# Kernel tuning notes

Measured on AMD Instinct MI355X. Metric: run time of the kernel, lower is better.

## Reference

```python
import jax, jax.numpy as jnp
import numpy as np

B, L, HID = 4, 1024, 1024
H, D = 16, 64  # num heads, head size


def setup_inputs() -> dict:
    key = jax.random.key(0)
    ks = jax.random.split(key, 12)
    s = 0.02
    return {
        "hidden_states": jax.random.normal(ks[0], (B, L, HID), jnp.float32),
        "attention_mask": jnp.zeros((B, 1, 1, L), jnp.float32),
        "structure_matrix": jax.random.normal(ks[1], (L, L, D), jnp.float32),
        # torch nn.Linear weights are [out, in]
        "Wq": jax.random.normal(ks[2], (H * D, HID), jnp.float32) * s,
        "bq": jnp.zeros((H * D,), jnp.float32),
        "Wk": jax.random.normal(ks[3], (H * D, HID), jnp.float32) * s,
        "bk": jnp.zeros((H * D,), jnp.float32),
        "Wv": jax.random.normal(ks[4], (H * D, HID), jnp.float32) * s,
        "bv": jnp.zeros((H * D,), jnp.float32),
        "Wsq": jax.random.normal(ks[5], (D, D), jnp.float32) * s,
        "bsq": jnp.zeros((D,), jnp.float32),
        "Wsk": jax.random.normal(ks[6], (D, D), jnp.float32) * s,
        "bsk": jnp.zeros((D,), jnp.float32),
    }


def _heads(x):
    # [B, L, H*D] -> [B, H, L, D]
    return x.reshape(B, L, H, D).transpose(0, 2, 1, 3)


def reference(hidden_states, attention_mask, structure_matrix,
              Wq, bq, Wk, bk, Wv, bv, Wsq, bsq, Wsk, bsk):
    q = _heads(hidden_states @ Wq.T + bq)  # [B,H,L,D]
    k = _heads(hidden_states @ Wk.T + bk)
    v = _heads(hidden_states @ Wv.T + bv)

    scores = jnp.einsum('bhld,bhrd->bhlr', q, k)

    sq = structure_matrix @ Wsq.T + bsq  # [L,L,D]
    sk = structure_matrix @ Wsk.T + bsk
    scores = scores + jnp.einsum('bhld,lrd->bhlr', q, sq) \
                    + jnp.einsum('bhrd,lrd->bhlr', k, sk)

    scores = scores / jnp.sqrt(jnp.float32(D)) + attention_mask
    probs = jax.nn.softmax(scores, axis=-1)
    ctx = jnp.einsum('bhlr,bhrd->bhld', probs, v)
    ctx = ctx.transpose(0, 2, 1, 3).reshape(B, L, H * D)
    return ctx, scores
```

## Files before the change

kernel.cpp:

```cpp
#include <hip/hip_runtime.h>

typedef __attribute__((ext_vector_type(8))) short short8v;
typedef __attribute__((ext_vector_type(4))) short short4v;
typedef __attribute__((ext_vector_type(4))) float float4v;

#define MFMA16(a,b,c) __builtin_amdgcn_mfma_f32_16x16x32_bf16(a,b,c,0,0,0)

__device__ __forceinline__ unsigned short f2b(float f) {
    union { float f; unsigned u; } v; v.f = f;
    unsigned r = v.u + 0x7FFFu + ((v.u >> 16) & 1u);
    return (unsigned short)(r >> 16);
}
__device__ __forceinline__ float b2f(unsigned short s) {
    union { unsigned u; float f; } v; v.u = ((unsigned)s) << 16;
    return v.f;
}
__device__ __forceinline__ short8v pack8(float4v a, float4v b) {
    union { unsigned u[4]; short8v s; } o;
    asm("v_cvt_pk_bf16_f32 %0, %1, %2" : "=v"(o.u[0]) : "v"(a[0]), "v"(a[1]));
    asm("v_cvt_pk_bf16_f32 %0, %1, %2" : "=v"(o.u[1]) : "v"(a[2]), "v"(a[3]));
    asm("v_cvt_pk_bf16_f32 %0, %1, %2" : "=v"(o.u[2]) : "v"(b[0]), "v"(b[1]));
    asm("v_cvt_pk_bf16_f32 %0, %1, %2" : "=v"(o.u[3]) : "v"(b[2]), "v"(b[3]));
    return o.s;
}

__global__ __launch_bounds__(256) void pack_all(
    const float* __restrict__ hidden, const float* __restrict__ Wq,
    const float* __restrict__ Wk, const float* __restrict__ Wv,
    unsigned short* __restrict__ hb, unsigned short* __restrict__ Wqb,
    unsigned short* __restrict__ Wkb, unsigned short* __restrict__ Wvb) {
    const int bid = blockIdx.x;
    const float* in; unsigned short* out; int i;
    if (bid < 2048)      { in = hidden; out = hb;  i = bid * 256 + threadIdx.x; }
    else if (bid < 2560) { in = Wq; out = Wqb; i = (bid - 2048) * 256 + threadIdx.x; }
    else if (bid < 3072) { in = Wk; out = Wkb; i = (bid - 2560) * 256 + threadIdx.x; }
    else                 { in = Wv; out = Wvb; i = (bid - 3072) * 256 + threadIdx.x; }
    float4v a = *(const float4v*)&in[(size_t)i * 8];
    float4v b = *(const float4v*)&in[(size_t)i * 8 + 4];
    *(short8v*)&out[(size_t)i * 8] = pack8(a, b);
}

__global__ __launch_bounds__(256) void qkv_gemm(
    const unsigned short* __restrict__ A,
    const unsigned short* __restrict__ W,
    const float* __restrict__ bias,
    unsigned short* __restrict__ out, int vmode) {
    const int wave = threadIdx.x >> 6, lane = threadIdx.x & 63;
    const int m0 = blockIdx.y * 128 + wave * 32;
    const int n0 = blockIdx.x * 64;
    const int lrow = lane & 15, g8 = (lane >> 4) << 3, row4 = (lane >> 4) << 2;
    float4v acc[2][4] = {};
    const unsigned short* Ap = A + (size_t)(m0 + lrow) * 1024 + g8;
    const unsigned short* Wp = W + (size_t)(n0 + lrow) * 1024 + g8;
#pragma unroll 2
    for (int k0 = 0; k0 < 1024; k0 += 32) {
        short8v a0 = *(const short8v*)(Ap + k0);
        short8v a1 = *(const short8v*)(Ap + 16 * 1024 + k0);
        short8v b0 = *(const short8v*)(Wp + k0);
        short8v b1 = *(const short8v*)(Wp + 16 * 1024 + k0);
        short8v b2 = *(const short8v*)(Wp + 32 * 1024 + k0);
        short8v b3 = *(const short8v*)(Wp + 48 * 1024 + k0);
        acc[0][0] = MFMA16(a0, b0, acc[0][0]); acc[0][1] = MFMA16(a0, b1, acc[0][1]);
        acc[0][2] = MFMA16(a0, b2, acc[0][2]); acc[0][3] = MFMA16(a0, b3, acc[0][3]);
        acc[1][0] = MFMA16(a1, b0, acc[1][0]); acc[1][1] = MFMA16(a1, b1, acc[1][1]);
        acc[1][2] = MFMA16(a1, b2, acc[1][2]); acc[1][3] = MFMA16(a1, b3, acc[1][3]);
    }
#pragma unroll
    for (int nt = 0; nt < 4; ++nt) {
        const int n = n0 + nt * 16 + lrow;
        const float bz = bias[n];
        const int h = n >> 6, d = n & 63;
#pragma unroll
        for (int mt = 0; mt < 2; ++mt) {
            const int mb = m0 + mt * 16 + row4;
            if (vmode == 0) {
#pragma unroll
                for (int j = 0; j < 4; ++j) {
                    const int m = mb + j;
                    const int b = m >> 10, l = m & 1023;
                    out[(((size_t)(b * 16 + h) << 10) + l) * 64 + d] = f2b(acc[mt][nt][j] + bz);
                }
            } else {
                const int b = mb >> 10, r = mb & 1023;
                short4v pk;
#pragma unroll
                for (int j = 0; j < 4; ++j) pk[j] = (short)f2b(acc[mt][nt][j] + bz);
                *(short4v*)&out[((((size_t)(b * 16 + h)) << 6) + d) * 1024 + r] = pk;
            }
        }
    }
}

__global__ __launch_bounds__(256) void headproj(
    const unsigned short* __restrict__ xh,
    const float* __restrict__ Wsx,
    const float* __restrict__ bsx,
    unsigned short* __restrict__ x2b,
    float* __restrict__ xbv) {
    __shared__ __align__(16) float Ws[64 * 64];
    __shared__ float bs[64];
    __shared__ __align__(16) unsigned short Xl[64 * 64];
    const int tid = threadIdx.x;
    const int l = blockIdx.x;
#pragma unroll
    for (int i = 0; i < 4; ++i)
        *(float4v*)&Ws[tid * 4 + i * 1024] = *(const float4v*)&Wsx[tid * 4 + i * 1024];
    if (tid < 64) bs[tid] = bsx[tid];
    {
        const int bhh = tid >> 2, dq = (tid & 3) * 16;
        const unsigned short* src = &xh[((size_t)bhh * 1024 + l) * 64 + dq];
        *(short8v*)&Xl[bhh * 64 + dq] = *(const short8v*)src;
        *(short8v*)&Xl[bhh * 64 + dq + 8] = *(const short8v*)(src + 8);
    }
    __syncthreads();
    const int bh = tid >> 2, e0 = (tid & 3) * 16;
    float acc[16] = {};
    float bacc = 0.f;
    for (int d = 0; d < 64; ++d) {
        const float xd = b2f(Xl[bh * 64 + d]);
        bacc += xd * bs[d];
        const float* wr = &Ws[d * 64 + e0];
#pragma unroll
        for (int e = 0; e < 16; e += 4) {
            float4v w = *(const float4v*)&wr[e];
            acc[e] += xd * w[0]; acc[e + 1] += xd * w[1];
            acc[e + 2] += xd * w[2]; acc[e + 3] += xd * w[3];
        }
    }
    short8v p0, p1;
#pragma unroll
    for (int e = 0; e < 8; ++e) { p0[e] = (short)f2b(acc[e]); p1[e] = (short)f2b(acc[e + 8]); }
    unsigned short* dst = &x2b[((size_t)l * 64 + bh) * 64 + e0];
    *(short8v*)dst = p0; *(short8v*)(dst + 8) = p1;
    if ((tid & 3) == 0) xbv[l * 64 + bh] = bacc;
}

__global__ __launch_bounds__(256, 2) void struct_fused(
    const float* __restrict__ S,
    const unsigned short* __restrict__ q2b,
    const unsigned short* __restrict__ k2b,
    const float* __restrict__ qbv,
    const float* __restrict__ kbv,
    unsigned short* __restrict__ sb) {
    __shared__ __align__(16) float Ssh[256 * 64];
    __shared__ __align__(16) unsigned short t3g[4][4][16][16];
    const int tid = threadIdx.x;
    const int w = tid >> 6, lane = tid & 63;
    const int lrow = lane & 15, g = lane >> 4;
    const int g8 = g << 3, row4 = g << 2;
    const int w16 = w << 4;
    const int r0 = blockIdx.x << 4, l0 = blockIdx.y << 4;

    {
        const int rowoff = lane >> 4, c = lane & 15;
#pragma unroll
        for (int i = 0; i < 16; ++i) {
            const int row = (w << 6) + (i << 2) + rowoff;
            const int key = (row ^ (row >> 4)) & 7;
            const int sc = ((((c >> 1) ^ key) << 1) | (c & 1));
            const float* src =
                S + ((size_t)(l0 + (row >> 4)) * 1024 + r0 + (row & 15)) * 64 + (sc << 2);
            float* dst = Ssh + (size_t)((w << 6) + (i << 2)) * 64;
            __builtin_amdgcn_global_load_lds(
                (const __attribute__((address_space(1))) void*)src,
                (__attribute__((address_space(3))) void*)dst, 16, 0, 0);
        }
    }
    float kbreg[4];
#pragma unroll
    for (int j = 0; j < 4; ++j)
        kbreg[j] = kbv[(size_t)(r0 + row4 + j) * 64 + w16 + lrow];
    asm volatile("s_waitcnt vmcnt(0)" ::: "memory");
    __syncthreads();

    float4v c3[16];
#pragma unroll
    for (int ri = 0; ri < 16; ++ri) {
        const int row = lrow * 16 + ri;
        const int key = (lrow ^ ri) & 7;
        const float* pr = Ssh + row * 64;
        const int p0 = (g ^ key) << 3, p1 = ((4 + g) ^ key) << 3;
        short8v a0 = pack8(*(const float4v*)(pr + p0), *(const float4v*)(pr + p0 + 4));
        short8v a1 = pack8(*(const float4v*)(pr + p1), *(const float4v*)(pr + p1 + 4));
        const unsigned short* Bp = k2b + ((size_t)(r0 + ri) * 64 + w16 + lrow) * 64 + g8;
        short8v b0 = *(const short8v*)Bp;
        short8v b1 = *(const short8v*)(Bp + 32);
        float4v acc = {};
        acc = MFMA16(a0, b0, acc);
        acc = MFMA16(a1, b1, acc);
        c3[ri] = acc;
    }

#pragma unroll
    for (int G = 0; G < 4; ++G) {
        if (g == G) {
#pragma unroll
            for (int j = 0; j < 4; ++j) {
                short8v lo, hi;
                float4v la{c3[0][j], c3[1][j], c3[2][j], c3[3][j]};
                float4v lb{c3[4][j], c3[5][j], c3[6][j], c3[7][j]};
                float4v ha{c3[8][j], c3[9][j], c3[10][j], c3[11][j]};
                float4v hb{c3[12][j], c3[13][j], c3[14][j], c3[15][j]};
                lo = pack8(la, lb); hi = pack8(ha, hb);
                *(short8v*)&t3g[w][j][lrow][0] = lo;
                *(short8v*)&t3g[w][j][lrow][8] = hi;
            }
        }
        asm volatile("s_waitcnt lgkmcnt(0)" ::: "memory");
#pragma unroll
        for (int lj = 0; lj < 4; ++lj) {
            const int li = (G << 2) + lj;
            const int row = li * 16 + lrow;
            const int key = (li ^ lrow) & 7;
            const float* pr = Ssh + row * 64;
            const int p0 = (g ^ key) << 3, p1 = ((4 + g) ^ key) << 3;
            short8v a0 = pack8(*(const float4v*)(pr + p0), *(const float4v*)(pr + p0 + 4));
            short8v a1 = pack8(*(const float4v*)(pr + p1), *(const float4v*)(pr + p1 + 4));
            const unsigned short* Bp = q2b + ((size_t)(l0 + li) * 64 + w16 + lrow) * 64 + g8;
            short8v b0 = *(const short8v*)Bp;
            short8v b1 = *(const short8v*)(Bp + 32);
            float4v c2 = {};
            c2 = MFMA16(a0, b0, c2);
            c2 = MFMA16(a1, b1, c2);
            short4v t3v = *(const short4v*)&t3g[w][lj][lrow][row4];
            const float qb = qbv[(size_t)(l0 + li) * 64 + w16 + lrow];
            short4v outv;
#pragma unroll
            for (int j = 0; j < 4; ++j)
                outv[j] = (short)f2b(c2[j] + b2f((unsigned short)t3v[j]) + qb + kbreg[j]);
            *(short4v*)&sb[((size_t)(l0 + li) * 64 + w16 + lrow) * 1024 + r0 + row4] = outv;
        }
    }
}

__global__ __launch_bounds__(256) void flash_kernel(
    const unsigned short* __restrict__ qh,
    const unsigned short* __restrict__ kh,
    const unsigned short* __restrict__ vT,
    const unsigned short* __restrict__ sb,
    const float* __restrict__ mask,
    float* __restrict__ scores,
    float* __restrict__ ctx) {
    __shared__ __align__(16) float scL[32 * 64];
    __shared__ __align__(16) unsigned short pL[32 * 64];
    __shared__ float mL[32], sL[32], fL[32];
    const int bid = blockIdx.x;
    const int virt = (bid & 7) * 256 + (bid >> 3);
    const int bh = virt >> 5, lt = virt & 31;
    const int b = bh >> 4, h = bh & 15, l0 = lt * 32;
    const int tid = threadIdx.x, wave = tid >> 6, lane = tid & 63;
    const int lrow = lane & 15, g8 = (lane >> 4) << 3, row4 = (lane >> 4) << 2;
    short8v qf[2][2];
#pragma unroll
    for (int mt = 0; mt < 2; ++mt)
#pragma unroll
        for (int ks = 0; ks < 2; ++ks)
            qf[mt][ks] = *(const short8v*)&qh[((size_t)bh * 1024 + l0 + mt * 16 + lrow) * 64 + ks * 32 + g8];
    float4v opv[2] = {};
    if (tid < 32) { mL[tid] = -3e38f; sL[tid] = 0.f; }
    __syncthreads();
    const int tl = tid >> 3, tr8 = tid & 7;
    const int keyS = ((tl >> 2) & 3) << 4;
    const int keyP = (tl & 7) << 3;
    for (int rt = 0; rt < 16; ++rt) {
        const int r0 = rt * 64;
        float4v sacc[2] = {};
#pragma unroll
        for (int ks = 0; ks < 2; ++ks) {
            short8v kf = *(const short8v*)&kh[((size_t)bh * 1024 + r0 + wave * 16 + lrow) * 64 + ks * 32 + g8];
            sacc[0] = MFMA16(qf[0][ks], kf, sacc[0]);
            sacc[1] = MFMA16(qf[1][ks], kf, sacc[1]);
        }
#pragma unroll
        for (int mt = 0; mt < 2; ++mt)
#pragma unroll
            for (int j = 0; j < 4; ++j) {
                const int ll = mt * 16 + row4 + j;
                const int cc = wave * 16 + lrow;
                scL[ll * 64 + (cc ^ (((ll >> 2) & 3) << 4))] = sacc[mt][j];
            }
        __syncthreads();
        float4v x0 = *(const float4v*)&scL[tl * 64 + ((tr8 * 8) ^ keyS)];
        float4v x1 = *(const float4v*)&scL[tl * 64 + ((tr8 * 8 + 4) ^ keyS)];
        short8v sbv = *(const short8v*)&sb[((size_t)(l0 + tl) * 64 + bh) * 1024 + r0 + tr8 * 8];
        float4v mk0 = *(const float4v*)&mask[(size_t)b * 1024 + r0 + tr8 * 8];
        float4v mk1 = *(const float4v*)&mask[(size_t)b * 1024 + r0 + tr8 * 8 + 4];
        float s8[8];
#pragma unroll
        for (int i = 0; i < 4; ++i) {
            s8[i]     = (x0[i] + b2f((unsigned short)sbv[i])) * 0.125f + mk0[i];
            s8[i + 4] = (x1[i] + b2f((unsigned short)sbv[i + 4])) * 0.125f + mk1[i];
        }
        {
            float4v o0, o1;
#pragma unroll
            for (int i = 0; i < 4; ++i) { o0[i] = s8[i]; o1[i] = s8[i + 4]; }
            float* sgp = &scores[((size_t)bh * 1024 + l0 + tl) * 1024 + r0 + tr8 * 8];
            *(float4v*)sgp = o0; *(float4v*)(sgp + 4) = o1;
        }
        float tm = s8[0];
#pragma unroll
        for (int i = 1; i < 8; ++i) tm = fmaxf(tm, s8[i]);
        tm = fmaxf(tm, __shfl_xor(tm, 1));
        tm = fmaxf(tm, __shfl_xor(tm, 2));
        tm = fmaxf(tm, __shfl_xor(tm, 4));
        const float mold = mL[tl];
        const float mnew = fmaxf(mold, tm);
        const float f = __expf(mold - mnew);
        float psum = 0.f;
        float p8[8];
#pragma unroll
        for (int i = 0; i < 8; ++i) { p8[i] = __expf(s8[i] - mnew); psum += p8[i]; }
        psum += __shfl_xor(psum, 1);
        psum += __shfl_xor(psum, 2);
        psum += __shfl_xor(psum, 4);
        if (tr8 == 0) { sL[tl] = sL[tl] * f + psum; mL[tl] = mnew; fL[tl] = f; }
        short8v pk;
#pragma unroll
        for (int i = 0; i < 8; ++i) pk[i] = (short)f2b(p8[i]);
        *(short8v*)&pL[tl * 64 + ((tr8 * 8) ^ keyP)] = pk;
        __syncthreads();
#pragma unroll
        for (int mt = 0; mt < 2; ++mt)
#pragma unroll
            for (int j = 0; j < 4; ++j) opv[mt][j] *= fL[mt * 16 + row4 + j];
#pragma unroll
        for (int ks = 0; ks < 2; ++ks) {
            short8v pf0 = *(const short8v*)&pL[(lrow) * 64 + ((ks * 32 + g8) ^ ((lrow & 7) << 3))];
            short8v pf1 = *(const short8v*)&pL[(16 + lrow) * 64 + ((ks * 32 + g8) ^ ((lrow & 7) << 3))];
            short8v vf = *(const short8v*)&vT[((size_t)bh * 64 + wave * 16 + lrow) * 1024 + r0 + ks * 32 + g8];
            opv[0] = MFMA16(pf0, vf, opv[0]);
            opv[1] = MFMA16(pf1, vf, opv[1]);
        }
    }
#pragma unroll
    for (int mt = 0; mt < 2; ++mt)
#pragma unroll
        for (int j = 0; j < 4; ++j) {
            const int l = mt * 16 + row4 + j;
            const float inv = 1.f / sL[l];
            const int d = wave * 16 + lrow;
            ctx[((size_t)b * 1024 + l0 + l) * 1024 + h * 64 + d] = opv[mt][j] * inv;
        }
}

extern "C" void kernel_launch(void* const* d_in, const int* in_sizes, int n_in,
                              void* d_out, int out_size, void* d_ws, size_t ws_size,
                              hipStream_t stream) {
    (void)in_sizes; (void)n_in; (void)out_size; (void)ws_size;
    const float* hidden = (const float*)d_in[0];
    const float* mask   = (const float*)d_in[1];
    const float* S      = (const float*)d_in[2];
    const float* Wq  = (const float*)d_in[3];  const float* bq  = (const float*)d_in[4];
    const float* Wk  = (const float*)d_in[5];  const float* bk  = (const float*)d_in[6];
    const float* Wv  = (const float*)d_in[7];  const float* bv  = (const float*)d_in[8];
    const float* Wsq = (const float*)d_in[9];  const float* bsq = (const float*)d_in[10];
    const float* Wsk = (const float*)d_in[11]; const float* bsk = (const float*)d_in[12];

    float* ctx    = (float*)d_out;
    float* scores = ctx + (size_t)4 * 1024 * 1024;

    char* ws = (char*)d_ws;
    unsigned short* sbuf = (unsigned short*)ws;
    unsigned short* hb  = (unsigned short*)ws;
    unsigned short* Wqb = (unsigned short*)(ws + (8u << 20));
    unsigned short* Wkb = (unsigned short*)(ws + (10u << 20));
    unsigned short* Wvb = (unsigned short*)(ws + (12u << 20));
    unsigned short* qh  = (unsigned short*)(ws + (size_t)(128u) * 1024 * 1024);
    unsigned short* kh  = qh  + (size_t)4 * 1024 * 1024;
    unsigned short* vT  = kh  + (size_t)4 * 1024 * 1024;
    unsigned short* q2b = vT  + (size_t)4 * 1024 * 1024;
    unsigned short* k2b = q2b + (size_t)4 * 1024 * 1024;
    float* qbv = (float*)(k2b + (size_t)4 * 1024 * 1024);
    float* kbv = qbv + 65536;

    pack_all<<<3584, 256, 0, stream>>>(hidden, Wq, Wk, Wv, hb, Wqb, Wkb, Wvb);
    qkv_gemm<<<dim3(16, 32), 256, 0, stream>>>(hb, Wqb, bq, qh, 0);
    qkv_gemm<<<dim3(16, 32), 256, 0, stream>>>(hb, Wkb, bk, kh, 0);
    qkv_gemm<<<dim3(16, 32), 256, 0, stream>>>(hb, Wvb, bv, vT, 1);
    headproj<<<1024, 256, 0, stream>>>(qh, Wsq, bsq, q2b, qbv);
    headproj<<<1024, 256, 0, stream>>>(kh, Wsk, bsk, k2b, kbv);
    struct_fused<<<dim3(64, 64), 256, 0, stream>>>(S, q2b, k2b, qbv, kbv, sbuf);
    flash_kernel<<<2048, 256, 0, stream>>>(qh, kh, vT, sbuf, mask, scores, ctx);
}
```

Baseline: 535.9 us.

## Stage structure tile in LDS as bf16 via registers to raise occupancy

The structure-matrix tile now goes from global memory into registers, is converted to bf16 once, and is stored into shared memory with the same XOR swizzle. This replaces the direct fp32 global-to-LDS copy and the repeated fp32-to-bf16 packing at every MFMA operand read. Halving the LDS footprint lets launch bounds request 4 blocks per CU instead of 2. In exchange, the async LDS load path is lost and 16 float4 registers are held per thread during staging, which may raise register pressure.

```diff
diff --git a/kernel.cpp b/kernel.cpp
--- a/kernel.cpp
+++ b/kernel.cpp
@@ -3,6 +3,7 @@
 typedef __attribute__((ext_vector_type(8))) short short8v;
 typedef __attribute__((ext_vector_type(4))) short short4v;
 typedef __attribute__((ext_vector_type(4))) float float4v;
+typedef __attribute__((ext_vector_type(2))) unsigned int uint2v;
 
 #define MFMA16(a,b,c) __builtin_amdgcn_mfma_f32_16x16x32_bf16(a,b,c,0,0,0)
 
@@ -135,14 +136,14 @@
     if ((tid & 3) == 0) xbv[l * 64 + bh] = bacc;
 }
 
-__global__ __launch_bounds__(256, 2) void struct_fused(
+__global__ __launch_bounds__(256, 4) void struct_fused(
     const float* __restrict__ S,
     const unsigned short* __restrict__ q2b,
     const unsigned short* __restrict__ k2b,
     const float* __restrict__ qbv,
     const float* __restrict__ kbv,
     unsigned short* __restrict__ sb) {
-    __shared__ __align__(16) float Ssh[256 * 64];
+    __shared__ __align__(16) unsigned short Ssh[256 * 64];
     __shared__ __align__(16) unsigned short t3g[4][4][16][16];
     const int tid = threadIdx.x;
     const int w = tid >> 6, lane = tid & 63;
@@ -152,25 +153,27 @@
     const int r0 = blockIdx.x << 4, l0 = blockIdx.y << 4;
 
     {
-        const int rowoff = lane >> 4, c = lane & 15;
+        const int u = tid & 15, roff = tid >> 4;
+        const float* gp = S + ((size_t)l0 * 1024 + r0 + roff) * 64 + u * 4;
+        float4v f[16];
+#pragma unroll
+        for (int i = 0; i < 16; ++i)
+            f[i] = *(const float4v*)(gp + (size_t)i * 65536);
 #pragma unroll
         for (int i = 0; i < 16; ++i) {
-            const int row = (w << 6) + (i << 2) + rowoff;
-            const int key = (row ^ (row >> 4)) & 7;
-            const int sc = ((((c >> 1) ^ key) << 1) | (c & 1));
-            const float* src =
-                S + ((size_t)(l0 + (row >> 4)) * 1024 + r0 + (row & 15)) * 64 + (sc << 2);
-            float* dst = Ssh + (size_t)((w << 6) + (i << 2)) * 64;
-            __builtin_amdgcn_global_load_lds(
-                (const __attribute__((address_space(1))) void*)src,
-                (__attribute__((address_space(3))) void*)dst, 16, 0, 0);
+            const int R = (i << 4) + roff;
+            const int K3 = (roff ^ i) & 7;
+            const int pu = u ^ (K3 << 1);
+            union { unsigned uu[2]; uint2v v2; } o;
+            asm("v_cvt_pk_bf16_f32 %0, %1, %2" : "=v"(o.uu[0]) : "v"(f[i][0]), "v"(f[i][1]));
+            asm("v_cvt_pk_bf16_f32 %0, %1, %2" : "=v"(o.uu[1]) : "v"(f[i][2]), "v"(f[i][3]));
+            *(uint2v*)&Ssh[(R << 6) + (pu << 2)] = o.v2;
         }
     }
     float kbreg[4];
 #pragma unroll
     for (int j = 0; j < 4; ++j)
         kbreg[j] = kbv[(size_t)(r0 + row4 + j) * 64 + w16 + lrow];
-    asm volatile("s_waitcnt vmcnt(0)" ::: "memory");
     __syncthreads();
 
     float4v c3[16];
@@ -178,10 +181,8 @@
     for (int ri = 0; ri < 16; ++ri) {
         const int row = lrow * 16 + ri;
         const int key = (lrow ^ ri) & 7;
-        const float* pr = Ssh + row * 64;
-        const int p0 = (g ^ key) << 3, p1 = ((4 + g) ^ key) << 3;
-        short8v a0 = pack8(*(const float4v*)(pr + p0), *(const float4v*)(pr + p0 + 4));
-        short8v a1 = pack8(*(const float4v*)(pr + p1), *(const float4v*)(pr + p1 + 4));
+        short8v a0 = *(const short8v*)&Ssh[row * 64 + ((g ^ key) << 3)];
+        short8v a1 = *(const short8v*)&Ssh[row * 64 + (((4 + g) ^ key) << 3)];
         const unsigned short* Bp = k2b + ((size_t)(r0 + ri) * 64 + w16 + lrow) * 64 + g8;
         short8v b0 = *(const short8v*)Bp;
         short8v b1 = *(const short8v*)(Bp + 32);
@@ -196,14 +197,12 @@
         if (g == G) {
 #pragma unroll
             for (int j = 0; j < 4; ++j) {
-                short8v lo, hi;
                 float4v la{c3[0][j], c3[1][j], c3[2][j], c3[3][j]};
                 float4v lb{c3[4][j], c3[5][j], c3[6][j], c3[7][j]};
                 float4v ha{c3[8][j], c3[9][j], c3[10][j], c3[11][j]};
                 float4v hb{c3[12][j], c3[13][j], c3[14][j], c3[15][j]};
-                lo = pack8(la, lb); hi = pack8(ha, hb);
-                *(short8v*)&t3g[w][j][lrow][0] = lo;
-                *(short8v*)&t3g[w][j][lrow][8] = hi;
+                *(short8v*)&t3g[w][j][lrow][0] = pack8(la, lb);
+                *(short8v*)&t3g[w][j][lrow][8] = pack8(ha, hb);
             }
         }
         asm volatile("s_waitcnt lgkmcnt(0)" ::: "memory");
@@ -212,10 +211,8 @@
             const int li = (G << 2) + lj;
             const int row = li * 16 + lrow;
             const int key = (li ^ lrow) & 7;
-            const float* pr = Ssh + row * 64;
-            const int p0 = (g ^ key) << 3, p1 = ((4 + g) ^ key) << 3;
-            short8v a0 = pack8(*(const float4v*)(pr + p0), *(const float4v*)(pr + p0 + 4));
-            short8v a1 = pack8(*(const float4v*)(pr + p1), *(const float4v*)(pr + p1 + 4));
+            short8v a0 = *(const short8v*)&Ssh[row * 64 + ((g ^ key) << 3)];
+            short8v a1 = *(const short8v*)&Ssh[row * 64 + (((4 + g) ^ key) << 3)];
             const unsigned short* Bp = q2b + ((size_t)(l0 + li) * 64 + w16 + lrow) * 64 + g8;
             short8v b0 = *(const short8v*)Bp;
             short8v b1 = *(const short8v*)(Bp + 32);
```

After: 541.7 us. No clear change (+1.1%).
